# Performance work log

Measured on AMD Instinct MI355X. Metric: run time of the kernel, lower is better.

The kernel has to match this reference:

```python
import jax, jax.numpy as jnp
import numpy as np

NCLS, NDF, B = 256, 512, 1024
ALP = 0.1


def setup_inputs() -> dict:
    key = jax.random.key(0)
    k1, k2, k3 = jax.random.split(key, 3)
    df = jax.random.normal(k1, (B, NDF), dtype=jnp.float32)
    gt = jax.random.randint(k2, (B,), 0, NCLS)
    fc = jax.random.normal(k3, (NCLS, NDF), dtype=jnp.float32)
    return {"df": df, "gt": gt, "fc": fc}


def _update_stats(df, gt):
    """Sequential per-sample running mean/var update (moving_avg=False branch).
    Faithful to the torch no_grad loop: per-class counter `it`, c1=it/(it+1),
    c2=1/(it+1); mean[t]=f when it==0 else mean[t]*c1+f*c2;
    var[t]=var[t]*c1 + (f-mean[t])**2 * c1*c2. Buffers start at zero.
    """
    mean0 = jnp.zeros((NCLS, NDF), jnp.float32)
    var0 = jnp.zeros((NCLS, NDF), jnp.float32)
    it0 = jnp.zeros((NCLS,), jnp.int32)

    def step(carry, xt):
        mean, var, it = carry
        f, t = xt
        n = it[t]
        nf = n.astype(jnp.float32)
        c1 = nf / (nf + 1.0)
        c2 = 1.0 / (nf + 1.0)
        m_t = jnp.where(n == 0, f, mean[t] * c1 + f * c2)
        a = (f - m_t) ** 2
        v_t = var[t] * c1 + a * c1 * c2
        return (mean.at[t].set(m_t), var.at[t].set(v_t), it.at[t].add(1)), None

    (mean, var, it), _ = jax.lax.scan(step, (mean0, var0, it0), (df, gt))
    return mean, var


def reference(df, gt, fc):
    # stats updated from detached features (torch uses no_grad)
    _, var = _update_stats(jax.lax.stop_gradient(df), gt)
    Var = var[gt]          # (B, ndf)
    Fc = fc[gt]            # (B, ndf): column of fc for each sample's class
    W = fc[None, :, :] - Fc[:, None, :]  # (B, ncls, ndf)
    # score[b,c] = W[b,c,:].df[b,:] + alp/2 * (W**2)[b,c,:].Var[b,:]
    score = jnp.einsum('bcd,bd->bc', W, df) \
        + 0.5 * ALP * jnp.einsum('bcd,bd->bc', W * W, Var)
    return score[:, :, None]  # (B, ncls, 1), matching torch matmul output
```

## Files before the change

### kernel.cpp

```cpp
#include <hip/hip_runtime.h>

#define NCLS 256
#define NDF  512
#define BSZ  1024
#define ALP  0.1f


typedef __attribute__((ext_vector_type(8))) short bf16x8;
typedef __attribute__((ext_vector_type(4))) float f32x4;

__device__ __forceinline__ unsigned rne_pk(float lo, float hi) {
    union { float f; unsigned u; } a, b;
    a.f = lo; b.f = hi;
    unsigned ua = (a.u + 0x7FFFu + ((a.u >> 16) & 1u)) >> 16;
    unsigned ub = (b.u + 0x7FFFu + ((b.u >> 16) & 1u)) & 0xFFFF0000u;
    return ua | ub;
}
__device__ __forceinline__ uint4 pk16(float4 p, float4 q) {
    uint4 r;
    r.x = rne_pk(p.x, p.y); r.y = rne_pk(p.z, p.w);
    r.z = rne_pk(q.x, q.y); r.w = rne_pk(q.z, q.w);
    return r;
}
__device__ __forceinline__ float bf16r(float x) {
    union { float f; unsigned u; } c; c.f = x;
    c.u = (c.u + 0x7FFFu + ((c.u >> 16) & 1u)) & 0xFFFF0000u;
    return c.f;
}

__global__ __launch_bounds__(256) void k1_R_bias(const float* __restrict__ df,
                                                 const int* __restrict__ gt,
                                                 const float* __restrict__ fc,
                                                 float* __restrict__ Rp,
                                                 float* __restrict__ bias1) {
    __shared__ union {
        struct { alignas(16) char A[64 * 256]; alignas(16) char B[64 * 256]; } g;
        struct { int gts[BSZ]; unsigned long long bmap[64 * 16]; } r;
    } sm;

    const int tid = threadIdx.x;
    const int bid = blockIdx.x;
    const int lane = tid & 63;

    if (bid >= 128) {
        const int b = (bid - 128) * 4 + (tid >> 6);
        const int t = gt[b];
        const float* pd = df + b * NDF + lane * 8;
        const float* pf = fc + t * NDF + lane * 8;
        const float4 d0 = ((const float4*)pd)[0], d1 = ((const float4*)pd)[1];
        const float4 f0 = ((const float4*)pf)[0], f1 = ((const float4*)pf)[1];
        float s = 0.f;
        s = fmaf(bf16r(d0.x), bf16r(f0.x), s); s = fmaf(bf16r(d0.y), bf16r(f0.y), s);
        s = fmaf(bf16r(d0.z), bf16r(f0.z), s); s = fmaf(bf16r(d0.w), bf16r(f0.w), s);
        s = fmaf(bf16r(d1.x), bf16r(f1.x), s); s = fmaf(bf16r(d1.y), bf16r(f1.y), s);
        s = fmaf(bf16r(d1.z), bf16r(f1.z), s); s = fmaf(bf16r(d1.w), bf16r(f1.w), s);
#pragma unroll
        for (int off = 32; off; off >>= 1) s += __shfl_xor(s, off, 64);
        if (lane == 0) bias1[b] = s;
        return;
    }

    const int wv = tid >> 6;
    const int wm = (wv >> 1) * 32, wn = (wv & 1) * 32;
    const int fr = lane & 15;
    const int fkb = (lane >> 4) * 16;
    const int fswz = (fr & 7) << 4;

    const int sr = tid >> 2;
    const int sswz = (sr & 7) << 4;
    char* arow = sm.g.A + sr * 256;
    char* brow = sm.g.B + sr * 256;

    f32x4 acc[2][2];
    acc[0][0] = 0.f; acc[0][1] = 0.f; acc[1][0] = 0.f; acc[1][1] = 0.f;

    auto mma_step = [&](int k0b) {
        const int kb = (k0b + fkb) ^ fswz;
        const bf16x8 aF0 = *(const bf16x8*)(sm.g.A + (wm + fr) * 256 + kb);
        const bf16x8 aF1 = *(const bf16x8*)(sm.g.A + (wm + 16 + fr) * 256 + kb);
        const bf16x8 bF0 = *(const bf16x8*)(sm.g.B + (wn + fr) * 256 + kb);
        const bf16x8 bF1 = *(const bf16x8*)(sm.g.B + (wn + 16 + fr) * 256 + kb);
        acc[0][0] = __builtin_amdgcn_mfma_f32_16x16x32_bf16(aF0, bF0, acc[0][0], 0, 0, 0);
        acc[0][1] = __builtin_amdgcn_mfma_f32_16x16x32_bf16(aF0, bF1, acc[0][1], 0, 0, 0);
        acc[1][0] = __builtin_amdgcn_mfma_f32_16x16x32_bf16(aF1, bF0, acc[1][0], 0, 0, 0);
        acc[1][1] = __builtin_amdgcn_mfma_f32_16x16x32_bf16(aF1, bF1, acc[1][1], 0, 0, 0);
    };

    const int z = bid & 7;
    const int tile = bid >> 3;
    const int bm = tile & 3, bn = tile >> 2;
    const int D0 = z * 64;
    const int clocal = sr;
    const int myclass = bm * 64 + clocal;
    const int dim0 = D0 + (tid & 3) * 16;
    const int kbl = (tid & 3) * 32;
    const int kbq = 128 + kbl;

    const float* Bg = fc + (bn * 64 + sr) * NDF + dim0;
    const float4 b0 = ((const float4*)Bg)[0], b1 = ((const float4*)Bg)[1],
                 b2 = ((const float4*)Bg)[2], b3 = ((const float4*)Bg)[3];

    for (int i = tid; i < BSZ; i += 256) sm.r.gts[i] = gt[i];
    for (int i = tid; i < 1024; i += 256) sm.r.bmap[i] = 0ull;
    __syncthreads();
    for (int i = tid; i < BSZ; i += 256) {
        const int c = sm.r.gts[i] - bm * 64;
        if ((unsigned)c < 64u) atomicOr(&sm.r.bmap[c * 16 + (i >> 6)], 1ull << (i & 63));
    }
    const float* fct = fc + myclass * NDF + dim0;
    float fcq[16];
    {
        const float4 q0 = ((const float4*)fct)[0], q1 = ((const float4*)fct)[1];
        const float4 q2 = ((const float4*)fct)[2], q3 = ((const float4*)fct)[3];
        fcq[0]=q0.x; fcq[1]=q0.y; fcq[2]=q0.z; fcq[3]=q0.w;
        fcq[4]=q1.x; fcq[5]=q1.y; fcq[6]=q1.z; fcq[7]=q1.w;
        fcq[8]=q2.x; fcq[9]=q2.y; fcq[10]=q2.z; fcq[11]=q2.w;
        fcq[12]=q3.x; fcq[13]=q3.y; fcq[14]=q3.z; fcq[15]=q3.w;
    }
    __syncthreads();

    float m[16], v[16];
#pragma unroll
    for (int j = 0; j < 16; ++j) { m[j] = 0.f; v[j] = 0.f; }
    float nf = 0.f;
    {
        int w = 0;
        unsigned long long bits = sm.r.bmap[clocal * 16];
        auto next = [&]() -> int {
            while (bits == 0ull) {
                if (w >= 15) return -1;
                bits = sm.r.bmap[clocal * 16 + (++w)];
            }
            const int b = __ffsll((unsigned long long)bits) - 1;
            bits &= bits - 1ull;
            return (w << 6) + b;
        };
        int cur = next();
        float f[16];
        if (cur >= 0) {
            const float* p = df + cur * NDF + dim0;
            const float4 q0 = ((const float4*)p)[0], q1 = ((const float4*)p)[1];
            const float4 q2 = ((const float4*)p)[2], q3 = ((const float4*)p)[3];
            f[0]=q0.x; f[1]=q0.y; f[2]=q0.z; f[3]=q0.w;
            f[4]=q1.x; f[5]=q1.y; f[6]=q1.z; f[7]=q1.w;
            f[8]=q2.x; f[9]=q2.y; f[10]=q2.z; f[11]=q2.w;
            f[12]=q3.x; f[13]=q3.y; f[14]=q3.z; f[15]=q3.w;
        }
        while (cur >= 0) {
            const int nxt = next();
            float g[16];
            if (nxt >= 0) {
                const float* p = df + nxt * NDF + dim0;
                const float4 q0 = ((const float4*)p)[0], q1 = ((const float4*)p)[1];
                const float4 q2 = ((const float4*)p)[2], q3 = ((const float4*)p)[3];
                g[0]=q0.x; g[1]=q0.y; g[2]=q0.z; g[3]=q0.w;
                g[4]=q1.x; g[5]=q1.y; g[6]=q1.z; g[7]=q1.w;
                g[8]=q2.x; g[9]=q2.y; g[10]=q2.z; g[11]=q2.w;
                g[12]=q3.x; g[13]=q3.y; g[14]=q3.z; g[15]=q3.w;
            }
            const float c2 = 1.0f / (nf + 1.0f);
            const float c1 = nf * c2;
            const float c12 = c1 * c2;
#pragma unroll
            for (int j = 0; j < 16; ++j) {
                m[j] = m[j] * c1 + f[j] * c2;
                const float a = f[j] - m[j];
                v[j] = v[j] * c1 + a * a * c12;
            }
            nf += 1.0f;
#pragma unroll
            for (int j = 0; j < 16; ++j) f[j] = g[j];
            cur = nxt;
        }
    }
    __syncthreads();

    {
        float4 l0, l1, l2, l3;
        l0.x=-2.f*fcq[0]*v[0];  l0.y=-2.f*fcq[1]*v[1];  l0.z=-2.f*fcq[2]*v[2];  l0.w=-2.f*fcq[3]*v[3];
        l1.x=-2.f*fcq[4]*v[4];  l1.y=-2.f*fcq[5]*v[5];  l1.z=-2.f*fcq[6]*v[6];  l1.w=-2.f*fcq[7]*v[7];
        l2.x=-2.f*fcq[8]*v[8];  l2.y=-2.f*fcq[9]*v[9];  l2.z=-2.f*fcq[10]*v[10]; l2.w=-2.f*fcq[11]*v[11];
        l3.x=-2.f*fcq[12]*v[12]; l3.y=-2.f*fcq[13]*v[13]; l3.z=-2.f*fcq[14]*v[14]; l3.w=-2.f*fcq[15]*v[15];
        float4 p0, p1, p2, p3;
        p0.x=v[0];  p0.y=v[1];  p0.z=v[2];  p0.w=v[3];
        p1.x=v[4];  p1.y=v[5];  p1.z=v[6];  p1.w=v[7];
        p2.x=v[8];  p2.y=v[9];  p2.z=v[10]; p2.w=v[11];
        p3.x=v[12]; p3.y=v[13]; p3.z=v[14]; p3.w=v[15];
        float4 s0, s1, s2, s3;
        s0.x=b0.x*b0.x; s0.y=b0.y*b0.y; s0.z=b0.z*b0.z; s0.w=b0.w*b0.w;
        s1.x=b1.x*b1.x; s1.y=b1.y*b1.y; s1.z=b1.z*b1.z; s1.w=b1.w*b1.w;
        s2.x=b2.x*b2.x; s2.y=b2.y*b2.y; s2.z=b2.z*b2.z; s2.w=b2.w*b2.w;
        s3.x=b3.x*b3.x; s3.y=b3.y*b3.y; s3.z=b3.z*b3.z; s3.w=b3.w*b3.w;
        *(uint4*)(arow + ((kbl + 0) ^ sswz)) = pk16(l0, l1);
        *(uint4*)(arow + ((kbl + 16) ^ sswz)) = pk16(l2, l3);
        *(uint4*)(arow + ((kbq + 0) ^ sswz)) = pk16(p0, p1);
        *(uint4*)(arow + ((kbq + 16) ^ sswz)) = pk16(p2, p3);
        *(uint4*)(brow + ((kbl + 0) ^ sswz)) = pk16(b0, b1);
        *(uint4*)(brow + ((kbl + 16) ^ sswz)) = pk16(b2, b3);
        *(uint4*)(brow + ((kbq + 0) ^ sswz)) = pk16(s0, s1);
        *(uint4*)(brow + ((kbq + 16) ^ sswz)) = pk16(s2, s3);
    }
    __syncthreads();
    mma_step(0); mma_step(64); mma_step(128); mma_step(192);

    float* base = Rp + z * (NCLS * NCLS) + (bm * 64) * NCLS + bn * 64;
#pragma unroll
    for (int mi = 0; mi < 2; ++mi)
#pragma unroll
        for (int ni = 0; ni < 2; ++ni)
#pragma unroll
            for (int r2 = 0; r2 < 4; ++r2)
                base[(wm + mi * 16 + (lane >> 4) * 4 + r2) * NCLS + wn + ni * 16 + fr] =
                    acc[mi][ni][r2];
}

__global__ __launch_bounds__(256, 2) void k2_s1_out(const float* __restrict__ df,
                                                    const int* __restrict__ gt,
                                                    const float* __restrict__ fc,
                                                    const float* __restrict__ Rp,
                                                    const float* __restrict__ bias1,
                                                    float* __restrict__ out) {
    __shared__ alignas(16) char A[32 * 1024];
    __shared__ alignas(16) char B[32 * 1024];

    const int tid = threadIdx.x;
    const int bn = blockIdx.x & 7, bm = blockIdx.x >> 3;

    const int row = tid >> 3, kc = tid & 7;
    const float* Ag = df + (bm * 32 + row) * NDF + kc * 64;
    const float* Bg = fc + (bn * 32 + row) * NDF + kc * 64;
    float4 a[16], b[16];
#pragma unroll
    for (int i = 0; i < 16; ++i) a[i] = ((const float4*)Ag)[i];
#pragma unroll
    for (int i = 0; i < 16; ++i) b[i] = ((const float4*)Bg)[i];
    const int swz = (row & 7) << 4;
    char* ar = A + row * 1024;
    char* br = B + row * 1024;
#pragma unroll
    for (int i = 0; i < 8; ++i)
        *(uint4*)(ar + ((kc * 128 + i * 16) ^ swz)) = pk16(a[2 * i], a[2 * i + 1]);
#pragma unroll
    for (int i = 0; i < 8; ++i)
        *(uint4*)(br + ((kc * 128 + i * 16) ^ swz)) = pk16(b[2 * i], b[2 * i + 1]);
    __syncthreads();

    const int lane = tid & 63;
    const int wv = tid >> 6;
    const int wm = (wv >> 1) * 16, wn = (wv & 1) * 16;
    const int fr = lane & 15;
    const int fkb = (lane >> 4) * 16;
    const int fswz = (fr & 7) << 4;
    f32x4 accE = 0.f, accO = 0.f;
#pragma unroll
    for (int s = 0; s < 16; s += 2) {
        const int kb0 = (s * 64 + fkb) ^ fswz;
        const int kb1 = ((s + 1) * 64 + fkb) ^ fswz;
        const bf16x8 aF0 = *(const bf16x8*)(A + (wm + fr) * 1024 + kb0);
        const bf16x8 bF0 = *(const bf16x8*)(B + (wn + fr) * 1024 + kb0);
        const bf16x8 aF1 = *(const bf16x8*)(A + (wm + fr) * 1024 + kb1);
        const bf16x8 bF1 = *(const bf16x8*)(B + (wn + fr) * 1024 + kb1);
        accE = __builtin_amdgcn_mfma_f32_16x16x32_bf16(aF0, bF0, accE, 0, 0, 0);
        accO = __builtin_amdgcn_mfma_f32_16x16x32_bf16(aF1, bF1, accO, 0, 0, 0);
    }

    const int colg = bn * 32 + wn + fr;
#pragma unroll
    for (int r = 0; r < 4; ++r) {
        const int bg = bm * 32 + wm + (lane >> 4) * 4 + r;
        const int t = gt[bg];
        float vR = 0.f, vtt = 0.f;
#pragma unroll
        for (int z = 0; z < 8; ++z) {
            const float* rp = Rp + z * (NCLS * NCLS) + t * NCLS;
            vR += rp[colg];
            vtt += rp[t];
        }
        const float v1 = accE[r] + accO[r] - bias1[bg];
        out[bg * NCLS + colg] = v1 + 0.5f * ALP * (vR - vtt);
    }
}

extern "C" void kernel_launch(void* const* d_in, const int* in_sizes, int n_in,
                              void* d_out, int out_size, void* d_ws, size_t ws_size,
                              hipStream_t stream) {
    const float* df = (const float*)d_in[0];
    const int* gt = (const int*)d_in[1];
    const float* fc = (const float*)d_in[2];
    float* out = (float*)d_out;

    float* ws = (float*)d_ws;
    float* Rp = ws;
    float* bias1 = Rp + 8 * NCLS * NCLS;

    k1_R_bias<<<384, 256, 0, stream>>>(df, gt, fc, Rp, bias1);
    k2_s1_out<<<256, 256, 0, stream>>>(df, gt, fc, Rp, bias1, out);
}
```

Baseline: 24.95 us.

## Fuse producer and consumer kernels with an atomic completion counter

The two launches are merged into one persistent-style kernel. Blocks 0-127 compute the partial R tiles and bump a global done counter with release semantics. Blocks 128-383 do the df·fc GEMM tile and compute the per-row bias locally, then spin until all producers finish before reading Rp. This removes the second launch and overlaps the consumer GEMM with producer work, but adds a memset, a spin-wait, and a deadlock risk if consumer blocks fill the GPU before the producers are scheduled.

```diff
diff --git a/kernel.cpp b/kernel.cpp
--- a/kernel.cpp
+++ b/kernel.cpp
@@ -27,74 +27,123 @@
     c.u = (c.u + 0x7FFFu + ((c.u >> 16) & 1u)) & 0xFFFF0000u;
     return c.f;
 }
-
-__global__ __launch_bounds__(256) void k1_R_bias(const float* __restrict__ df,
-                                                 const int* __restrict__ gt,
-                                                 const float* __restrict__ fc,
-                                                 float* __restrict__ Rp,
-                                                 float* __restrict__ bias1) {
+__device__ __forceinline__ void agent_store_f(float* p, float v) {
+    __hip_atomic_store(p, v, __ATOMIC_RELAXED, __HIP_MEMORY_SCOPE_AGENT);
+}
+__device__ __forceinline__ float agent_load_f(const float* p) {
+    return __hip_atomic_load(p, __ATOMIC_RELAXED, __HIP_MEMORY_SCOPE_AGENT);
+}
+
+__global__ __launch_bounds__(256) void fused_pc(const float* __restrict__ df,
+                                                const int* __restrict__ gt,
+                                                const float* __restrict__ fc,
+                                                float* __restrict__ Rp,
+                                                unsigned int* __restrict__ done,
+                                                float* __restrict__ out) {
     __shared__ union {
+        struct { alignas(16) char A[32 * 1024]; alignas(16) char B[32 * 1024]; } s;
         struct { alignas(16) char A[64 * 256]; alignas(16) char B[64 * 256]; } g;
         struct { int gts[BSZ]; unsigned long long bmap[64 * 16]; } r;
     } sm;
+    __shared__ float biasL[32];
 
     const int tid = threadIdx.x;
     const int bid = blockIdx.x;
     const int lane = tid & 63;
-
-    if (bid >= 128) {
-        const int b = (bid - 128) * 4 + (tid >> 6);
-        const int t = gt[b];
-        const float* pd = df + b * NDF + lane * 8;
-        const float* pf = fc + t * NDF + lane * 8;
-        const float4 d0 = ((const float4*)pd)[0], d1 = ((const float4*)pd)[1];
-        const float4 f0 = ((const float4*)pf)[0], f1 = ((const float4*)pf)[1];
-        float s = 0.f;
-        s = fmaf(bf16r(d0.x), bf16r(f0.x), s); s = fmaf(bf16r(d0.y), bf16r(f0.y), s);
-        s = fmaf(bf16r(d0.z), bf16r(f0.z), s); s = fmaf(bf16r(d0.w), bf16r(f0.w), s);
-        s = fmaf(bf16r(d1.x), bf16r(f1.x), s); s = fmaf(bf16r(d1.y), bf16r(f1.y), s);
-        s = fmaf(bf16r(d1.z), bf16r(f1.z), s); s = fmaf(bf16r(d1.w), bf16r(f1.w), s);
-#pragma unroll
-        for (int off = 32; off; off >>= 1) s += __shfl_xor(s, off, 64);
-        if (lane == 0) bias1[b] = s;
-        return;
-    }
-
     const int wv = tid >> 6;
-    const int wm = (wv >> 1) * 32, wn = (wv & 1) * 32;
     const int fr = lane & 15;
     const int fkb = (lane >> 4) * 16;
     const int fswz = (fr & 7) << 4;
 
-    const int sr = tid >> 2;
-    const int sswz = (sr & 7) << 4;
-    char* arow = sm.g.A + sr * 256;
-    char* brow = sm.g.B + sr * 256;
-
-    f32x4 acc[2][2];
-    acc[0][0] = 0.f; acc[0][1] = 0.f; acc[1][0] = 0.f; acc[1][1] = 0.f;
-
-    auto mma_step = [&](int k0b) {
-        const int kb = (k0b + fkb) ^ fswz;
-        const bf16x8 aF0 = *(const bf16x8*)(sm.g.A + (wm + fr) * 256 + kb);
-        const bf16x8 aF1 = *(const bf16x8*)(sm.g.A + (wm + 16 + fr) * 256 + kb);
-        const bf16x8 bF0 = *(const bf16x8*)(sm.g.B + (wn + fr) * 256 + kb);
-        const bf16x8 bF1 = *(const bf16x8*)(sm.g.B + (wn + 16 + fr) * 256 + kb);
-        acc[0][0] = __builtin_amdgcn_mfma_f32_16x16x32_bf16(aF0, bF0, acc[0][0], 0, 0, 0);
-        acc[0][1] = __builtin_amdgcn_mfma_f32_16x16x32_bf16(aF0, bF1, acc[0][1], 0, 0, 0);
-        acc[1][0] = __builtin_amdgcn_mfma_f32_16x16x32_bf16(aF1, bF0, acc[1][0], 0, 0, 0);
-        acc[1][1] = __builtin_amdgcn_mfma_f32_16x16x32_bf16(aF1, bF1, acc[1][1], 0, 0, 0);
-    };
+    if (bid >= 128) {
+        const int sid = bid - 128;
+        const int bm = sid >> 3, bn = sid & 7;
+        const int row = tid >> 3, kc = tid & 7, ln8 = tid & 7;
+
+        const float* Ag = df + (bm * 32 + row) * NDF + kc * 64;
+        const float* Bg = fc + (bn * 32 + row) * NDF + kc * 64;
+        float4 a[16], b[16];
+#pragma unroll
+        for (int i = 0; i < 16; ++i) a[i] = ((const float4*)Ag)[i];
+#pragma unroll
+        for (int i = 0; i < 16; ++i) b[i] = ((const float4*)Bg)[i];
+        const int swz = (row & 7) << 4;
+        char* ar = sm.s.A + row * 1024;
+        char* br = sm.s.B + row * 1024;
+#pragma unroll
+        for (int i = 0; i < 8; ++i)
+            *(uint4*)(ar + ((kc * 128 + i * 16) ^ swz)) = pk16(a[2 * i], a[2 * i + 1]);
+#pragma unroll
+        for (int i = 0; i < 8; ++i)
+            *(uint4*)(br + ((kc * 128 + i * 16) ^ swz)) = pk16(b[2 * i], b[2 * i + 1]);
+
+        const int trow = gt[bm * 32 + row];
+        const float* Tg = fc + trow * NDF + kc * 64;
+        float s = 0.f;
+#pragma unroll
+        for (int i = 0; i < 16; ++i) {
+            const float4 f = ((const float4*)Tg)[i];
+            s = fmaf(bf16r(a[i].x), bf16r(f.x), s);
+            s = fmaf(bf16r(a[i].y), bf16r(f.y), s);
+            s = fmaf(bf16r(a[i].z), bf16r(f.z), s);
+            s = fmaf(bf16r(a[i].w), bf16r(f.w), s);
+        }
+        s += __shfl_xor(s, 1); s += __shfl_xor(s, 2); s += __shfl_xor(s, 4);
+        if (ln8 == 0) biasL[row] = s;
+        __syncthreads();
+
+        const int wm = (wv >> 1) * 16, wn = (wv & 1) * 16;
+        f32x4 accE = 0.f, accO = 0.f;
+#pragma unroll
+        for (int st = 0; st < 16; st += 2) {
+            const int kb0 = (st * 64 + fkb) ^ fswz;
+            const int kb1 = ((st + 1) * 64 + fkb) ^ fswz;
+            const bf16x8 aF0 = *(const bf16x8*)(sm.s.A + (wm + fr) * 1024 + kb0);
+            const bf16x8 bF0 = *(const bf16x8*)(sm.s.B + (wn + fr) * 1024 + kb0);
+            const bf16x8 aF1 = *(const bf16x8*)(sm.s.A + (wm + fr) * 1024 + kb1);
+            const bf16x8 bF1 = *(const bf16x8*)(sm.s.B + (wn + fr) * 1024 + kb1);
+            accE = __builtin_amdgcn_mfma_f32_16x16x32_bf16(aF0, bF0, accE, 0, 0, 0);
+            accO = __builtin_amdgcn_mfma_f32_16x16x32_bf16(aF1, bF1, accO, 0, 0, 0);
+        }
+
+        if (tid == 0) {
+            while (__hip_atomic_load(done, __ATOMIC_ACQUIRE, __HIP_MEMORY_SCOPE_AGENT) < 128u)
+                __builtin_amdgcn_s_sleep(2);
+        }
+        __syncthreads();
+
+        const int colg = bn * 32 + wn + fr;
+#pragma unroll
+        for (int r = 0; r < 4; ++r) {
+            const int lrow = wm + (lane >> 4) * 4 + r;
+            const int bg = bm * 32 + lrow;
+            const int t = gt[bg];
+            float vR = 0.f, vtt = 0.f;
+#pragma unroll
+            for (int z = 0; z < 8; ++z) {
+                const float* rp = Rp + z * (NCLS * NCLS) + t * NCLS;
+                vR += agent_load_f(rp + colg);
+                vtt += agent_load_f(rp + t);
+            }
+            out[bg * NCLS + colg] = (accE[r] + accO[r] - biasL[lrow])
+                                    + 0.5f * ALP * (vR - vtt);
+        }
+        return;
+    }
 
     const int z = bid & 7;
     const int tile = bid >> 3;
     const int bm = tile & 3, bn = tile >> 2;
     const int D0 = z * 64;
+    const int sr = tid >> 2;
+    const int sswz = (sr & 7) << 4;
     const int clocal = sr;
     const int myclass = bm * 64 + clocal;
     const int dim0 = D0 + (tid & 3) * 16;
     const int kbl = (tid & 3) * 32;
     const int kbq = 128 + kbl;
+    char* arow = sm.g.A + sr * 256;
+    char* brow = sm.g.B + sr * 256;
 
     const float* Bg = fc + (bn * 64 + sr) * NDF + dim0;
     const float4 b0 = ((const float4*)Bg)[0], b1 = ((const float4*)Bg)[1],
@@ -201,7 +250,22 @@
         *(uint4*)(brow + ((kbq + 16) ^ sswz)) = pk16(s2, s3);
     }
     __syncthreads();
-    mma_step(0); mma_step(64); mma_step(128); mma_step(192);
+
+    const int wm = (wv >> 1) * 32, wn = (wv & 1) * 32;
+    f32x4 acc[2][2];
+    acc[0][0] = 0.f; acc[0][1] = 0.f; acc[1][0] = 0.f; acc[1][1] = 0.f;
+#pragma unroll
+    for (int st = 0; st < 4; ++st) {
+        const int kb = (st * 64 + fkb) ^ fswz;
+        const bf16x8 aF0 = *(const bf16x8*)(sm.g.A + (wm + fr) * 256 + kb);
+        const bf16x8 aF1 = *(const bf16x8*)(sm.g.A + (wm + 16 + fr) * 256 + kb);
+        const bf16x8 bF0 = *(const bf16x8*)(sm.g.B + (wn + fr) * 256 + kb);
+        const bf16x8 bF1 = *(const bf16x8*)(sm.g.B + (wn + 16 + fr) * 256 + kb);
+        acc[0][0] = __builtin_amdgcn_mfma_f32_16x16x32_bf16(aF0, bF0, acc[0][0], 0, 0, 0);
+        acc[0][1] = __builtin_amdgcn_mfma_f32_16x16x32_bf16(aF0, bF1, acc[0][1], 0, 0, 0);
+        acc[1][0] = __builtin_amdgcn_mfma_f32_16x16x32_bf16(aF1, bF0, acc[1][0], 0, 0, 0);
+        acc[1][1] = __builtin_amdgcn_mfma_f32_16x16x32_bf16(aF1, bF1, acc[1][1], 0, 0, 0);
+    }
 
     float* base = Rp + z * (NCLS * NCLS) + (bm * 64) * NCLS + bn * 64;
 #pragma unroll
@@ -210,75 +274,11 @@
         for (int ni = 0; ni < 2; ++ni)
 #pragma unroll
             for (int r2 = 0; r2 < 4; ++r2)
-                base[(wm + mi * 16 + (lane >> 4) * 4 + r2) * NCLS + wn + ni * 16 + fr] =
-                    acc[mi][ni][r2];
-}
-
-__global__ __launch_bounds__(256, 2) void k2_s1_out(const float* __restrict__ df,
-                                                    const int* __restrict__ gt,
-                                                    const float* __restrict__ fc,
-                                                    const float* __restrict__ Rp,
-                                                    const float* __restrict__ bias1,
-                                                    float* __restrict__ out) {
-    __shared__ alignas(16) char A[32 * 1024];
-    __shared__ alignas(16) char B[32 * 1024];
-
-    const int tid = threadIdx.x;
-    const int bn = blockIdx.x & 7, bm = blockIdx.x >> 3;
-
-    const int row = tid >> 3, kc = tid & 7;
-    const float* Ag = df + (bm * 32 + row) * NDF + kc * 64;
-    const float* Bg = fc + (bn * 32 + row) * NDF + kc * 64;
-    float4 a[16], b[16];
-#pragma unroll
-    for (int i = 0; i < 16; ++i) a[i] = ((const float4*)Ag)[i];
-#pragma unroll
-    for (int i = 0; i < 16; ++i) b[i] = ((const float4*)Bg)[i];
-    const int swz = (row & 7) << 4;
-    char* ar = A + row * 1024;
-    char* br = B + row * 1024;
-#pragma unroll
-    for (int i = 0; i < 8; ++i)
-        *(uint4*)(ar + ((kc * 128 + i * 16) ^ swz)) = pk16(a[2 * i], a[2 * i + 1]);
-#pragma unroll
-    for (int i = 0; i < 8; ++i)
-        *(uint4*)(br + ((kc * 128 + i * 16) ^ swz)) = pk16(b[2 * i], b[2 * i + 1]);
-    __syncthreads();
-
-    const int lane = tid & 63;
-    const int wv = tid >> 6;
-    const int wm = (wv >> 1) * 16, wn = (wv & 1) * 16;
-    const int fr = lane & 15;
-    const int fkb = (lane >> 4) * 16;
-    const int fswz = (fr & 7) << 4;
-    f32x4 accE = 0.f, accO = 0.f;
-#pragma unroll
-    for (int s = 0; s < 16; s += 2) {
-        const int kb0 = (s * 64 + fkb) ^ fswz;
-        const int kb1 = ((s + 1) * 64 + fkb) ^ fswz;
-        const bf16x8 aF0 = *(const bf16x8*)(A + (wm + fr) * 1024 + kb0);
-        const bf16x8 bF0 = *(const bf16x8*)(B + (wn + fr) * 1024 + kb0);
-        const bf16x8 aF1 = *(const bf16x8*)(A + (wm + fr) * 1024 + kb1);
-        const bf16x8 bF1 = *(const bf16x8*)(B + (wn + fr) * 1024 + kb1);
-        accE = __builtin_amdgcn_mfma_f32_16x16x32_bf16(aF0, bF0, accE, 0, 0, 0);
-        accO = __builtin_amdgcn_mfma_f32_16x16x32_bf16(aF1, bF1, accO, 0, 0, 0);
-    }
-
-    const int colg = bn * 32 + wn + fr;
-#pragma unroll
-    for (int r = 0; r < 4; ++r) {
-        const int bg = bm * 32 + wm + (lane >> 4) * 4 + r;
-        const int t = gt[bg];
-        float vR = 0.f, vtt = 0.f;
-#pragma unroll
-        for (int z = 0; z < 8; ++z) {
-            const float* rp = Rp + z * (NCLS * NCLS) + t * NCLS;
-            vR += rp[colg];
-            vtt += rp[t];
-        }
-        const float v1 = accE[r] + accO[r] - bias1[bg];
-        out[bg * NCLS + colg] = v1 + 0.5f * ALP * (vR - vtt);
-    }
+                agent_store_f(base + (wm + mi * 16 + (lane >> 4) * 4 + r2) * NCLS
+                                   + wn + ni * 16 + fr, acc[mi][ni][r2]);
+    __syncthreads();
+    if (tid == 0)
+        __hip_atomic_fetch_add(done, 1u, __ATOMIC_RELEASE, __HIP_MEMORY_SCOPE_AGENT);
 }
 
 extern "C" void kernel_launch(void* const* d_in, const int* in_sizes, int n_in,
@@ -291,8 +291,8 @@
 
     float* ws = (float*)d_ws;
     float* Rp = ws;
-    float* bias1 = Rp + 8 * NCLS * NCLS;
-
-    k1_R_bias<<<384, 256, 0, stream>>>(df, gt, fc, Rp, bias1);
-    k2_s1_out<<<256, 256, 0, stream>>>(df, gt, fc, Rp, bias1, out);
-}
+    unsigned int* done = (unsigned int*)(Rp + 8 * NCLS * NCLS);
+
+    hipMemsetAsync(done, 0, sizeof(unsigned int), stream);
+    fused_pc<<<384, 256, 0, stream>>>(df, gt, fc, Rp, done, out);
+}
```

Measured after the change: 62.70 us. 2.51x slower.

## Merge bias blocks into stats blocks and split K across waves in output kernel

Applied to the files above, without the earlier changes.

The first kernel drops its separate bias blocks. Each block now runs 512 threads: four waves do the per-class running-variance scan and the MFMA tile, and four extra waves compute the bias dot products for 8 samples during the scan. The second kernel moves to 512 threads and splits the K dimension across two wave halves, combining the partial MFMA accumulators through shared memory, so each thread issues fewer loads and MFMAs. This adds an extra shared-memory fold and two more barriers, and the larger blocks may change occupancy.

```diff
diff --git a/kernel.cpp b/kernel.cpp
--- a/kernel.cpp
+++ b/kernel.cpp
@@ -28,7 +28,7 @@
     return c.f;
 }
 
-__global__ __launch_bounds__(256) void k1_R_bias(const float* __restrict__ df,
+__global__ __launch_bounds__(512) void k1_R_bias(const float* __restrict__ df,
                                                  const int* __restrict__ gt,
                                                  const float* __restrict__ fc,
                                                  float* __restrict__ Rp,
@@ -41,89 +41,53 @@
     const int tid = threadIdx.x;
     const int bid = blockIdx.x;
     const int lane = tid & 63;
-
-    if (bid >= 128) {
-        const int b = (bid - 128) * 4 + (tid >> 6);
-        const int t = gt[b];
-        const float* pd = df + b * NDF + lane * 8;
-        const float* pf = fc + t * NDF + lane * 8;
-        const float4 d0 = ((const float4*)pd)[0], d1 = ((const float4*)pd)[1];
-        const float4 f0 = ((const float4*)pf)[0], f1 = ((const float4*)pf)[1];
-        float s = 0.f;
-        s = fmaf(bf16r(d0.x), bf16r(f0.x), s); s = fmaf(bf16r(d0.y), bf16r(f0.y), s);
-        s = fmaf(bf16r(d0.z), bf16r(f0.z), s); s = fmaf(bf16r(d0.w), bf16r(f0.w), s);
-        s = fmaf(bf16r(d1.x), bf16r(f1.x), s); s = fmaf(bf16r(d1.y), bf16r(f1.y), s);
-        s = fmaf(bf16r(d1.z), bf16r(f1.z), s); s = fmaf(bf16r(d1.w), bf16r(f1.w), s);
-#pragma unroll
-        for (int off = 32; off; off >>= 1) s += __shfl_xor(s, off, 64);
-        if (lane == 0) bias1[b] = s;
-        return;
-    }
-
     const int wv = tid >> 6;
-    const int wm = (wv >> 1) * 32, wn = (wv & 1) * 32;
-    const int fr = lane & 15;
-    const int fkb = (lane >> 4) * 16;
-    const int fswz = (fr & 7) << 4;
-
-    const int sr = tid >> 2;
-    const int sswz = (sr & 7) << 4;
-    char* arow = sm.g.A + sr * 256;
-    char* brow = sm.g.B + sr * 256;
-
-    f32x4 acc[2][2];
-    acc[0][0] = 0.f; acc[0][1] = 0.f; acc[1][0] = 0.f; acc[1][1] = 0.f;
-
-    auto mma_step = [&](int k0b) {
-        const int kb = (k0b + fkb) ^ fswz;
-        const bf16x8 aF0 = *(const bf16x8*)(sm.g.A + (wm + fr) * 256 + kb);
-        const bf16x8 aF1 = *(const bf16x8*)(sm.g.A + (wm + 16 + fr) * 256 + kb);
-        const bf16x8 bF0 = *(const bf16x8*)(sm.g.B + (wn + fr) * 256 + kb);
-        const bf16x8 bF1 = *(const bf16x8*)(sm.g.B + (wn + 16 + fr) * 256 + kb);
-        acc[0][0] = __builtin_amdgcn_mfma_f32_16x16x32_bf16(aF0, bF0, acc[0][0], 0, 0, 0);
-        acc[0][1] = __builtin_amdgcn_mfma_f32_16x16x32_bf16(aF0, bF1, acc[0][1], 0, 0, 0);
-        acc[1][0] = __builtin_amdgcn_mfma_f32_16x16x32_bf16(aF1, bF0, acc[1][0], 0, 0, 0);
-        acc[1][1] = __builtin_amdgcn_mfma_f32_16x16x32_bf16(aF1, bF1, acc[1][1], 0, 0, 0);
-    };
+
+    for (int i = tid; i < BSZ; i += 512) sm.r.gts[i] = gt[i];
+    for (int i = tid; i < 1024; i += 512) sm.r.bmap[i] = 0ull;
+    __syncthreads();
+    for (int i = tid; i < BSZ; i += 512) {
+        const int c = sm.r.gts[i] - ((bid >> 3) & 3) * 64;
+        if ((unsigned)c < 64u) atomicOr(&sm.r.bmap[c * 16 + (i >> 6)], 1ull << (i & 63));
+    }
 
     const int z = bid & 7;
     const int tile = bid >> 3;
     const int bm = tile & 3, bn = tile >> 2;
     const int D0 = z * 64;
+    const int sr = tid >> 2;
+    const int sswz = (sr & 7) << 4;
     const int clocal = sr;
-    const int myclass = bm * 64 + clocal;
+    const int myclass = bm * 64 + (clocal & 63);
     const int dim0 = D0 + (tid & 3) * 16;
     const int kbl = (tid & 3) * 32;
     const int kbq = 128 + kbl;
 
-    const float* Bg = fc + (bn * 64 + sr) * NDF + dim0;
-    const float4 b0 = ((const float4*)Bg)[0], b1 = ((const float4*)Bg)[1],
-                 b2 = ((const float4*)Bg)[2], b3 = ((const float4*)Bg)[3];
-
-    for (int i = tid; i < BSZ; i += 256) sm.r.gts[i] = gt[i];
-    for (int i = tid; i < 1024; i += 256) sm.r.bmap[i] = 0ull;
-    __syncthreads();
-    for (int i = tid; i < BSZ; i += 256) {
-        const int c = sm.r.gts[i] - bm * 64;
-        if ((unsigned)c < 64u) atomicOr(&sm.r.bmap[c * 16 + (i >> 6)], 1ull << (i & 63));
-    }
-    const float* fct = fc + myclass * NDF + dim0;
     float fcq[16];
-    {
+    float4 b0, b1, b2, b3;
+    int bsample = 0, bt = 0;
+    if (wv < 4) {
+        const float* Bg = fc + (bn * 64 + sr) * NDF + dim0;
+        b0 = ((const float4*)Bg)[0]; b1 = ((const float4*)Bg)[1];
+        b2 = ((const float4*)Bg)[2]; b3 = ((const float4*)Bg)[3];
+        const float* fct = fc + myclass * NDF + dim0;
         const float4 q0 = ((const float4*)fct)[0], q1 = ((const float4*)fct)[1];
         const float4 q2 = ((const float4*)fct)[2], q3 = ((const float4*)fct)[3];
         fcq[0]=q0.x; fcq[1]=q0.y; fcq[2]=q0.z; fcq[3]=q0.w;
         fcq[4]=q1.x; fcq[5]=q1.y; fcq[6]=q1.z; fcq[7]=q1.w;
         fcq[8]=q2.x; fcq[9]=q2.y; fcq[10]=q2.z; fcq[11]=q2.w;
         fcq[12]=q3.x; fcq[13]=q3.y; fcq[14]=q3.z; fcq[15]=q3.w;
+    } else {
+        bsample = bid * 8 + (wv - 4) * 2 + (lane >> 5);
+        bt = sm.r.gts[bsample];
     }
     __syncthreads();
 
     float m[16], v[16];
-#pragma unroll
-    for (int j = 0; j < 16; ++j) { m[j] = 0.f; v[j] = 0.f; }
-    float nf = 0.f;
-    {
+    if (wv < 4) {
+#pragma unroll
+        for (int j = 0; j < 16; ++j) { m[j] = 0.f; v[j] = 0.f; }
+        float nf = 0.f;
         int w = 0;
         unsigned long long bits = sm.r.bmap[clocal * 16];
         auto next = [&]() -> int {
@@ -172,10 +136,29 @@
             for (int j = 0; j < 16; ++j) f[j] = g[j];
             cur = nxt;
         }
-    }
-    __syncthreads();
-
-    {
+    } else {
+        const int l32 = lane & 31;
+        const float* pd = df + bsample * NDF + l32 * 16;
+        const float* pf = fc + bt * NDF + l32 * 16;
+        float s = 0.f;
+#pragma unroll
+        for (int i = 0; i < 4; ++i) {
+            const float4 dq = ((const float4*)pd)[i];
+            const float4 fq = ((const float4*)pf)[i];
+            s = fmaf(bf16r(dq.x), bf16r(fq.x), s);
+            s = fmaf(bf16r(dq.y), bf16r(fq.y), s);
+            s = fmaf(bf16r(dq.z), bf16r(fq.z), s);
+            s = fmaf(bf16r(dq.w), bf16r(fq.w), s);
+        }
+        s += __shfl_xor(s, 1); s += __shfl_xor(s, 2); s += __shfl_xor(s, 4);
+        s += __shfl_xor(s, 8); s += __shfl_xor(s, 16);
+        if (l32 == 0) bias1[bsample] = s;
+    }
+    __syncthreads();
+
+    if (wv < 4) {
+        char* arow = sm.g.A + sr * 256;
+        char* brow = sm.g.B + sr * 256;
         float4 l0, l1, l2, l3;
         l0.x=-2.f*fcq[0]*v[0];  l0.y=-2.f*fcq[1]*v[1];  l0.z=-2.f*fcq[2]*v[2];  l0.w=-2.f*fcq[3]*v[3];
         l1.x=-2.f*fcq[4]*v[4];  l1.y=-2.f*fcq[5]*v[5];  l1.z=-2.f*fcq[6]*v[6];  l1.w=-2.f*fcq[7]*v[7];
@@ -201,72 +184,97 @@
         *(uint4*)(brow + ((kbq + 16) ^ sswz)) = pk16(s2, s3);
     }
     __syncthreads();
-    mma_step(0); mma_step(64); mma_step(128); mma_step(192);
-
-    float* base = Rp + z * (NCLS * NCLS) + (bm * 64) * NCLS + bn * 64;
-#pragma unroll
-    for (int mi = 0; mi < 2; ++mi)
-#pragma unroll
-        for (int ni = 0; ni < 2; ++ni)
-#pragma unroll
-            for (int r2 = 0; r2 < 4; ++r2)
-                base[(wm + mi * 16 + (lane >> 4) * 4 + r2) * NCLS + wn + ni * 16 + fr] =
-                    acc[mi][ni][r2];
-}
-
-__global__ __launch_bounds__(256, 2) void k2_s1_out(const float* __restrict__ df,
-                                                    const int* __restrict__ gt,
-                                                    const float* __restrict__ fc,
-                                                    const float* __restrict__ Rp,
-                                                    const float* __restrict__ bias1,
-                                                    float* __restrict__ out) {
-    __shared__ alignas(16) char A[32 * 1024];
-    __shared__ alignas(16) char B[32 * 1024];
+
+    if (wv < 4) {
+        const int fr = lane & 15;
+        const int fkb = (lane >> 4) * 16;
+        const int fswz = (fr & 7) << 4;
+        const int wm = (wv >> 1) * 32, wn = (wv & 1) * 32;
+        f32x4 acc[2][2];
+        acc[0][0] = 0.f; acc[0][1] = 0.f; acc[1][0] = 0.f; acc[1][1] = 0.f;
+#pragma unroll
+        for (int st = 0; st < 4; ++st) {
+            const int kb = (st * 64 + fkb) ^ fswz;
+            const bf16x8 aF0 = *(const bf16x8*)(sm.g.A + (wm + fr) * 256 + kb);
+            const bf16x8 aF1 = *(const bf16x8*)(sm.g.A + (wm + 16 + fr) * 256 + kb);
+            const bf16x8 bF0 = *(const bf16x8*)(sm.g.B + (wn + fr) * 256 + kb);
+            const bf16x8 bF1 = *(const bf16x8*)(sm.g.B + (wn + 16 + fr) * 256 + kb);
+            acc[0][0] = __builtin_amdgcn_mfma_f32_16x16x32_bf16(aF0, bF0, acc[0][0], 0, 0, 0);
+            acc[0][1] = __builtin_amdgcn_mfma_f32_16x16x32_bf16(aF0, bF1, acc[0][1], 0, 0, 0);
+            acc[1][0] = __builtin_amdgcn_mfma_f32_16x16x32_bf16(aF1, bF0, acc[1][0], 0, 0, 0);
+            acc[1][1] = __builtin_amdgcn_mfma_f32_16x16x32_bf16(aF1, bF1, acc[1][1], 0, 0, 0);
+        }
+        float* base = Rp + z * (NCLS * NCLS) + (bm * 64) * NCLS + bn * 64;
+#pragma unroll
+        for (int mi = 0; mi < 2; ++mi)
+#pragma unroll
+            for (int ni = 0; ni < 2; ++ni)
+#pragma unroll
+                for (int r2 = 0; r2 < 4; ++r2)
+                    base[(wm + mi * 16 + (lane >> 4) * 4 + r2) * NCLS + wn + ni * 16 + fr] =
+                        acc[mi][ni][r2];
+    }
+}
+
+__global__ __launch_bounds__(512) void k2_s1_out(const float* __restrict__ df,
+                                                 const int* __restrict__ gt,
+                                                 const float* __restrict__ fc,
+                                                 const float* __restrict__ Rp,
+                                                 const float* __restrict__ bias1,
+                                                 float* __restrict__ out) {
+    __shared__ union {
+        struct { alignas(16) char A[32 * 1024]; alignas(16) char B[32 * 1024]; } t;
+        float fold[8 * 256];
+    } sm;
 
     const int tid = threadIdx.x;
     const int bn = blockIdx.x & 7, bm = blockIdx.x >> 3;
-
-    const int row = tid >> 3, kc = tid & 7;
-    const float* Ag = df + (bm * 32 + row) * NDF + kc * 64;
-    const float* Bg = fc + (bn * 32 + row) * NDF + kc * 64;
-    float4 a[16], b[16];
-#pragma unroll
-    for (int i = 0; i < 16; ++i) a[i] = ((const float4*)Ag)[i];
-#pragma unroll
-    for (int i = 0; i < 16; ++i) b[i] = ((const float4*)Bg)[i];
+    const int lane = tid & 63, wv = tid >> 6;
+
+    const int row = tid >> 4, seg = tid & 15;
+    const float* Ag = df + (bm * 32 + row) * NDF + seg * 32;
+    const float* Bg = fc + (bn * 32 + row) * NDF + seg * 32;
+    float4 a[8], b[8];
+#pragma unroll
+    for (int i = 0; i < 8; ++i) a[i] = ((const float4*)Ag)[i];
+#pragma unroll
+    for (int i = 0; i < 8; ++i) b[i] = ((const float4*)Bg)[i];
     const int swz = (row & 7) << 4;
-    char* ar = A + row * 1024;
-    char* br = B + row * 1024;
-#pragma unroll
-    for (int i = 0; i < 8; ++i)
-        *(uint4*)(ar + ((kc * 128 + i * 16) ^ swz)) = pk16(a[2 * i], a[2 * i + 1]);
-#pragma unroll
-    for (int i = 0; i < 8; ++i)
-        *(uint4*)(br + ((kc * 128 + i * 16) ^ swz)) = pk16(b[2 * i], b[2 * i + 1]);
-    __syncthreads();
-
-    const int lane = tid & 63;
-    const int wv = tid >> 6;
-    const int wm = (wv >> 1) * 16, wn = (wv & 1) * 16;
+    char* ar = sm.t.A + row * 1024;
+    char* br = sm.t.B + row * 1024;
+#pragma unroll
+    for (int j = 0; j < 4; ++j)
+        *(uint4*)(ar + ((seg * 64 + j * 16) ^ swz)) = pk16(a[2 * j], a[2 * j + 1]);
+#pragma unroll
+    for (int j = 0; j < 4; ++j)
+        *(uint4*)(br + ((seg * 64 + j * 16) ^ swz)) = pk16(b[2 * j], b[2 * j + 1]);
+    __syncthreads();
+
+    const int q = wv & 3, h = wv >> 2;
+    const int wm = (q >> 1) * 16, wn = (q & 1) * 16;
     const int fr = lane & 15;
     const int fkb = (lane >> 4) * 16;
     const int fswz = (fr & 7) << 4;
-    f32x4 accE = 0.f, accO = 0.f;
-#pragma unroll
-    for (int s = 0; s < 16; s += 2) {
-        const int kb0 = (s * 64 + fkb) ^ fswz;
-        const int kb1 = ((s + 1) * 64 + fkb) ^ fswz;
-        const bf16x8 aF0 = *(const bf16x8*)(A + (wm + fr) * 1024 + kb0);
-        const bf16x8 bF0 = *(const bf16x8*)(B + (wn + fr) * 1024 + kb0);
-        const bf16x8 aF1 = *(const bf16x8*)(A + (wm + fr) * 1024 + kb1);
-        const bf16x8 bF1 = *(const bf16x8*)(B + (wn + fr) * 1024 + kb1);
-        accE = __builtin_amdgcn_mfma_f32_16x16x32_bf16(aF0, bF0, accE, 0, 0, 0);
-        accO = __builtin_amdgcn_mfma_f32_16x16x32_bf16(aF1, bF1, accO, 0, 0, 0);
-    }
+    f32x4 acc = 0.f;
+#pragma unroll
+    for (int s = 0; s < 8; ++s) {
+        const int kb = ((h * 8 + s) * 64 + fkb) ^ fswz;
+        const bf16x8 aF = *(const bf16x8*)(sm.t.A + (wm + fr) * 1024 + kb);
+        const bf16x8 bF = *(const bf16x8*)(sm.t.B + (wn + fr) * 1024 + kb);
+        acc = __builtin_amdgcn_mfma_f32_16x16x32_bf16(aF, bF, acc, 0, 0, 0);
+    }
+    __syncthreads();
+    ((f32x4*)sm.fold)[wv * 64 + lane] = acc;
+    __syncthreads();
+    const f32x4 other = ((f32x4*)sm.fold)[(wv ^ 4) * 64 + lane];
+    acc += other;
 
     const int colg = bn * 32 + wn + fr;
 #pragma unroll
-    for (int r = 0; r < 4; ++r) {
+    for (int rr = 0; rr < 2; ++rr) {
+        const float av = h ? ((rr == 0) ? acc[2] : acc[3])
+                           : ((rr == 0) ? acc[0] : acc[1]);
+        const int r = h * 2 + rr;
         const int bg = bm * 32 + wm + (lane >> 4) * 4 + r;
         const int t = gt[bg];
         float vR = 0.f, vtt = 0.f;
@@ -276,8 +284,7 @@
             vR += rp[colg];
             vtt += rp[t];
         }
-        const float v1 = accE[r] + accO[r] - bias1[bg];
-        out[bg * NCLS + colg] = v1 + 0.5f * ALP * (vR - vtt);
+        out[bg * NCLS + colg] = (av - bias1[bg]) + 0.5f * ALP * (vR - vtt);
     }
 }
 
@@ -293,6 +300,6 @@
     float* Rp = ws;
     float* bias1 = Rp + 8 * NCLS * NCLS;
 
-    k1_R_bias<<<384, 256, 0, stream>>>(df, gt, fc, Rp, bias1);
-    k2_s1_out<<<256, 256, 0, stream>>>(df, gt, fc, Rp, bias1, out);
-}
+    k1_R_bias<<<128, 512, 0, stream>>>(df, gt, fc, Rp, bias1);
+    k2_s1_out<<<256, 512, 0, stream>>>(df, gt, fc, Rp, bias1, out);
+}
```

Result: no change. 25.34 us (+1.5%).
